# Kernel tuning notes

Hardware: AMD Instinct MI355X
Metric: run time of the kernel (lower is better)

Reference implementation:

```python
import jax, jax.numpy as jnp
import numpy as np

IN_FEATURES = 4096
OUT_FEATURES = 4096
NNZ = 1677722  # round(0.1 * 4096 * 4096)
N_TOKENS = 8192


def setup_inputs() -> dict:
    key = jax.random.key(0)
    k1, k2, k3, k4 = jax.random.split(key, 4)
    inputs = jax.random.normal(k1, (N_TOKENS, IN_FEATURES), dtype=jnp.float32)
    bound = 1.0 / IN_FEATURES ** 0.5
    weights = jax.random.uniform(k2, (NNZ,), minval=-bound, maxval=bound, dtype=jnp.float32)
    bias = jax.random.uniform(k3, (OUT_FEATURES,), minval=-bound, maxval=bound, dtype=jnp.float32)
    # COO indices: row (output) and col (input) indices, sampled like np.random.choice
    flat = jax.random.randint(k4, (NNZ,), 0, IN_FEATURES * OUT_FEATURES)
    row_ind = flat // IN_FEATURES
    col_ind = flat % IN_FEATURES
    indices = jnp.stack((row_ind, col_ind)).astype(jnp.int64)
    return {"inputs": inputs, "weights": weights, "bias": bias, "indices": indices}


def reference(inputs, weights, bias, indices):
    # Densify COO weight (duplicates are summed, matching torch coalesce/to_dense)
    dense_w = jnp.zeros((OUT_FEATURES, IN_FEATURES), dtype=weights.dtype)
    dense_w = dense_w.at[indices[0], indices[1]].add(weights)
    # output = (W @ x^T)^T + b  ==  x @ W^T + b
    out = jnp.einsum('ni,oi->no', inputs, dense_w) + bias
    return out
```

## Files before the change

### kernel.cpp

```cpp
#include <hip/hip_runtime.h>

#define M_TOK 8192
#define NF    4096
#define KF    4096
#define BK    64

typedef __attribute__((ext_vector_type(8))) short bf16x8;
typedef __attribute__((ext_vector_type(4))) float f32x4;
typedef __attribute__((ext_vector_type(2))) short s16x2;

__device__ __forceinline__ unsigned short f2bf(float f) {
    unsigned u = __builtin_bit_cast(unsigned, f);
    u += 0x7FFFu + ((u >> 16) & 1u);
    return (unsigned short)(u >> 16);
}

__device__ __forceinline__ float bf2f(unsigned short b) {
    unsigned u = ((unsigned)b) << 16;
    return __builtin_bit_cast(float, u);
}

__device__ __forceinline__ void load_lds16(const unsigned short* g, unsigned short* l) {
    __builtin_amdgcn_global_load_lds(
        (const __attribute__((address_space(1))) unsigned int*)g,
        (__attribute__((address_space(3))) unsigned int*)l,
        16, 0, 0);
}

__global__ void prep_zero_convx(const float4* __restrict__ X, ushort4* __restrict__ Xb,
                                uint4* __restrict__ Wb, int nx4, int nwb) {
    int i = blockIdx.x * blockDim.x + threadIdx.x;
    if (i < nwb) Wb[i] = (uint4){0u, 0u, 0u, 0u};
    if (i < nx4) {
        float4 v = X[i];
        ushort4 o;
        o.x = f2bf(v.x); o.y = f2bf(v.y); o.z = f2bf(v.z); o.w = f2bf(v.w);
        Xb[i] = o;
    }
}

__global__ void scatter_bf16(const int* __restrict__ idx, const float* __restrict__ w,
                             unsigned short* __restrict__ Wb, int nnz) {
    int t = blockIdx.x * blockDim.x + threadIdx.x;
    if (t >= nnz) return;
    int r = idx[t];
    int c = idx[nnz + t];
    size_t elem = (size_t)r * KF + c;
#if __has_builtin(__builtin_amdgcn_global_atomic_fadd_v2bf16)
    unsigned short wb = f2bf(w[t]);
    s16x2 val;
    if (elem & 1) { val[0] = 0; val[1] = (short)wb; }
    else          { val[0] = (short)wb; val[1] = 0; }
    __builtin_amdgcn_global_atomic_fadd_v2bf16(
        (__attribute__((address_space(1))) s16x2*)(Wb + (elem & ~(size_t)1)), val);
#else
    unsigned* addr = (unsigned*)(Wb + (elem & ~(size_t)1));
    float wf = w[t];
    unsigned old = __hip_atomic_load(addr, __ATOMIC_RELAXED, __HIP_MEMORY_SCOPE_AGENT), assumed;
    do {
        assumed = old;
        unsigned short cur = (elem & 1) ? (unsigned short)(assumed >> 16)
                                        : (unsigned short)(assumed & 0xffffu);
        unsigned short nw = f2bf(bf2f(cur) + wf);
        unsigned newv = (elem & 1) ? ((assumed & 0x0000ffffu) | ((unsigned)nw << 16))
                                   : ((assumed & 0xffff0000u) | (unsigned)nw);
        old = atomicCAS(addr, assumed, newv);
    } while (old != assumed);
#endif
}

__global__ __launch_bounds__(256) void gemm_bt_bias(
    const unsigned short* __restrict__ A,
    const unsigned short* __restrict__ B,
    const float* __restrict__ bias,
    float* __restrict__ C)
{
    __shared__ unsigned short As[128 * BK];
    __shared__ unsigned short Bs[128 * BK];

    const int tid  = threadIdx.x;
    const int lane = tid & 63;
    const int wave = tid >> 6;
    const int wm   = wave >> 1;
    const int wn   = wave & 1;
    const int bm   = blockIdx.x;
    const int bn   = blockIdx.y;

    f32x4 acc[4][4] = {};

    const int lr8 = lane >> 3;
    const int lp  = lane & 7;
    const int gc  = lp ^ lr8;

    const unsigned short* gA[4];
    const unsigned short* gB[4];
#pragma unroll
    for (int t = 0; t < 4; ++t) {
        int r = wave * 32 + t * 8 + lr8;
        gA[t] = A + (size_t)(bm * 128 + r) * KF + gc * 8;
        gB[t] = B + (size_t)(bn * 128 + r) * KF + gc * 8;
    }
    unsigned short* lA[4];
    unsigned short* lB[4];
#pragma unroll
    for (int t = 0; t < 4; ++t) {
        lA[t] = &As[(wave * 32 + t * 8) * BK];
        lB[t] = &Bs[(wave * 32 + t * 8) * BK];
    }

    const int fr   = lane & 15;
    const int quad = lane >> 4;
    int offA[4][2], offB[4][2];
#pragma unroll
    for (int i = 0; i < 4; ++i) {
        int rA = wm * 64 + i * 16 + fr;
        int rB = wn * 64 + i * 16 + fr;
#pragma unroll
        for (int s = 0; s < 2; ++s) {
            int c = s * 4 + quad;
            offA[i][s] = rA * BK + ((c ^ (rA & 7)) * 8);
            offB[i][s] = rB * BK + ((c ^ (rB & 7)) * 8);
        }
    }

    for (int k0 = 0; k0 < KF; k0 += BK) {
        __syncthreads();
#pragma unroll
        for (int t = 0; t < 4; ++t) load_lds16(gA[t], lA[t]);
#pragma unroll
        for (int t = 0; t < 4; ++t) load_lds16(gB[t], lB[t]);
#pragma unroll
        for (int t = 0; t < 4; ++t) { gA[t] += BK; gB[t] += BK; }
        __syncthreads();

#pragma unroll
        for (int s = 0; s < 2; ++s) {
            bf16x8 af[4], bfr[4];
#pragma unroll
            for (int i = 0; i < 4; ++i) af[i]  = *(const bf16x8*)&As[offA[i][s]];
#pragma unroll
            for (int j = 0; j < 4; ++j) bfr[j] = *(const bf16x8*)&Bs[offB[j][s]];
#pragma unroll
            for (int i = 0; i < 4; ++i)
#pragma unroll
                for (int j = 0; j < 4; ++j)
                    acc[i][j] = __builtin_amdgcn_mfma_f32_16x16x32_bf16(af[i], bfr[j], acc[i][j], 0, 0, 0);
        }
    }

    const int crow = bm * 128 + wm * 64;
    const int ccol = bn * 128 + wn * 64;
    const int c_l  = lane & 15;
    const int r_l  = (lane >> 4) * 4;
#pragma unroll
    for (int j = 0; j < 4; ++j) {
        int col = ccol + j * 16 + c_l;
        float bv = bias[col];
#pragma unroll
        for (int i = 0; i < 4; ++i) {
#pragma unroll
            for (int r = 0; r < 4; ++r)
                C[(size_t)(crow + i * 16 + r_l + r) * NF + col] = acc[i][j][r] + bv;
        }
    }
}

extern "C" void kernel_launch(void* const* d_in, const int* in_sizes, int n_in,
                              void* d_out, int out_size, void* d_ws, size_t ws_size,
                              hipStream_t stream) {
    const float* x    = (const float*)d_in[0];
    const float* w    = (const float*)d_in[1];
    const float* bias = (const float*)d_in[2];
    const int*   idx  = (const int*)d_in[3];
    float* out = (float*)d_out;
    const int nnz = in_sizes[1];

    unsigned short* Wb = (unsigned short*)d_ws;
    unsigned short* Xb = (unsigned short*)((char*)d_ws + (size_t)NF * KF * sizeof(unsigned short));

    const int nx4 = M_TOK * KF / 4;
    const int nwb = NF * KF * 2 / 16;

    prep_zero_convx<<<(nx4 + 255) / 256, 256, 0, stream>>>(
        (const float4*)x, (ushort4*)Xb, (uint4*)Wb, nx4, nwb);
    scatter_bf16<<<(nnz + 255) / 256, 256, 0, stream>>>(idx, w, Wb, nnz);
    gemm_bt_bias<<<dim3(M_TOK / 128, NF / 128), 256, 0, stream>>>(Xb, Wb, bias, out);
}
```

Baseline: 594.3 us.

## Rewrite GEMM as 256x256 tile, 8-wave, double-buffered LDS pipeline with block swizzle

Replaces the 128x128, 4-wave, single-buffered GEMM with a 256x256 tile computed by 8 waves, each holding 8x4 MFMA accumulators. Global-to-LDS loads for the next K tile are interleaved with MFMA work on the current buffer using explicit vmcnt waits, raw barriers and s_setprio. A grid swizzle is added for L2 locality. The aim is to hide load latency and raise arithmetic intensity, at the cost of 128KB LDS per block, heavy register pressure and fragile hand-written synchronization.

```diff
diff --git a/kernel.cpp b/kernel.cpp
--- a/kernel.cpp
+++ b/kernel.cpp
@@ -4,6 +4,7 @@
 #define NF    4096
 #define KF    4096
 #define BK    64
+#define NT    (KF / BK)
 
 typedef __attribute__((ext_vector_type(8))) short bf16x8;
 typedef __attribute__((ext_vector_type(4))) float f32x4;
@@ -26,6 +27,14 @@
         (__attribute__((address_space(3))) unsigned int*)l,
         16, 0, 0);
 }
+
+__device__ __forceinline__ void block_bar() {
+    asm volatile("" ::: "memory");
+    __builtin_amdgcn_s_barrier();
+    asm volatile("" ::: "memory");
+}
+
+#define VMCNT(n) asm volatile("s_waitcnt vmcnt(" #n ")" ::: "memory")
 
 __global__ void prep_zero_convx(const float4* __restrict__ X, ushort4* __restrict__ Xb,
                                 uint4* __restrict__ Wb, int nx4, int nwb) {
@@ -69,95 +78,147 @@
 #endif
 }
 
-__global__ __launch_bounds__(256) void gemm_bt_bias(
+__global__ __launch_bounds__(512, 2) void gemm_bt_bias(
     const unsigned short* __restrict__ A,
     const unsigned short* __restrict__ B,
     const float* __restrict__ bias,
     float* __restrict__ C)
 {
-    __shared__ unsigned short As[128 * BK];
-    __shared__ unsigned short Bs[128 * BK];
+    __shared__ unsigned short lds_u[65536];
+    char* const ldsb = (char*)lds_u;
 
     const int tid  = threadIdx.x;
     const int lane = tid & 63;
     const int wave = tid >> 6;
-    const int wm   = wave >> 1;
-    const int wn   = wave & 1;
-    const int bm   = blockIdx.x;
-    const int bn   = blockIdx.y;
-
-    f32x4 acc[4][4] = {};
-
-    const int lr8 = lane >> 3;
-    const int lp  = lane & 7;
-    const int gc  = lp ^ lr8;
-
-    const unsigned short* gA[4];
-    const unsigned short* gB[4];
-#pragma unroll
-    for (int t = 0; t < 4; ++t) {
-        int r = wave * 32 + t * 8 + lr8;
-        gA[t] = A + (size_t)(bm * 128 + r) * KF + gc * 8;
-        gB[t] = B + (size_t)(bn * 128 + r) * KF + gc * 8;
-    }
-    unsigned short* lA[4];
-    unsigned short* lB[4];
-#pragma unroll
-    for (int t = 0; t < 4; ++t) {
-        lA[t] = &As[(wave * 32 + t * 8) * BK];
-        lB[t] = &Bs[(wave * 32 + t * 8) * BK];
-    }
-
-    const int fr   = lane & 15;
-    const int quad = lane >> 4;
-    int offA[4][2], offB[4][2];
-#pragma unroll
-    for (int i = 0; i < 4; ++i) {
-        int rA = wm * 64 + i * 16 + fr;
-        int rB = wn * 64 + i * 16 + fr;
-#pragma unroll
-        for (int s = 0; s < 2; ++s) {
-            int c = s * 4 + quad;
-            offA[i][s] = rA * BK + ((c ^ (rA & 7)) * 8);
-            offB[i][s] = rB * BK + ((c ^ (rB & 7)) * 8);
-        }
-    }
-
-    for (int k0 = 0; k0 < KF; k0 += BK) {
-        __syncthreads();
-#pragma unroll
-        for (int t = 0; t < 4; ++t) load_lds16(gA[t], lA[t]);
-#pragma unroll
-        for (int t = 0; t < 4; ++t) load_lds16(gB[t], lB[t]);
-#pragma unroll
-        for (int t = 0; t < 4; ++t) { gA[t] += BK; gB[t] += BK; }
-        __syncthreads();
-
-#pragma unroll
-        for (int s = 0; s < 2; ++s) {
-            bf16x8 af[4], bfr[4];
-#pragma unroll
-            for (int i = 0; i < 4; ++i) af[i]  = *(const bf16x8*)&As[offA[i][s]];
-#pragma unroll
-            for (int j = 0; j < 4; ++j) bfr[j] = *(const bf16x8*)&Bs[offB[j][s]];
-#pragma unroll
-            for (int i = 0; i < 4; ++i)
-#pragma unroll
-                for (int j = 0; j < 4; ++j)
-                    acc[i][j] = __builtin_amdgcn_mfma_f32_16x16x32_bf16(af[i], bfr[j], acc[i][j], 0, 0, 0);
-        }
-    }
-
-    const int crow = bm * 128 + wm * 64;
-    const int ccol = bn * 128 + wn * 64;
-    const int c_l  = lane & 15;
-    const int r_l  = (lane >> 4) * 4;
+    const int wm   = wave >> 2;
+    const int wn   = wave & 3;
+
+    const int flat = blockIdx.y * 32 + blockIdx.x;
+    const int swz  = (flat & 7) * 64 + (flat >> 3);
+    const int bm   = swz & 31;
+    const int bn   = swz >> 5;
+
+    f32x4 acc[8][4] = {};
+
+    const int gc   = (lane & 3) ^ ((lane >> 3) & 3);
+    const int srow = wave * 16 + (lane >> 2);
+    const unsigned short* gA   = A + (size_t)(bm * 256 + srow) * KF + gc * 8;
+    const unsigned short* gB   = B + (size_t)(bn * 256 + srow) * KF + gc * 8;
+    const unsigned short* gAHi = gA + (size_t)128 * KF;
+    const unsigned short* gBHi = gB + (size_t)128 * KF;
+
+    unsigned short* const sdus = lds_u + wave * 512;
+
+    const int fr    = lane & 15;
+    const int quad  = lane >> 4;
+    const int pos16 = (quad ^ ((fr >> 1) & 3)) << 4;
+    const int rdA   = (wm * 128 + fr) * 64 + pos16;
+    const int rdB   = 32768 + (wn * 64 + fr) * 64 + pos16;
+
+#define STAGE(gp, gpHi, region, pbuf, h) do { \
+    load_lds16((gp)   + (h) * 32, sdus + (((pbuf) * 65536 + (region) + (h) * 16384       ) >> 1)); \
+    load_lds16((gpHi) + (h) * 32, sdus + (((pbuf) * 65536 + (region) + (h) * 16384 + 8192) >> 1)); \
+} while (0)
+
+#define RD_A4(dst, pbuf, h, i0) do { \
+    _Pragma("unroll") \
+    for (int _i = 0; _i < 4; ++_i) \
+        dst[_i] = *(const bf16x8*)(ldsb + (pbuf) * 65536 + (h) * 16384 + rdA + ((i0) + _i) * 1024); \
+} while (0)
+
+#define RD_B4(dst, pbuf, h) do { \
+    _Pragma("unroll") \
+    for (int _j = 0; _j < 4; ++_j) \
+        dst[_j] = *(const bf16x8*)(ldsb + (pbuf) * 65536 + (h) * 16384 + rdB + _j * 1024); \
+} while (0)
+
+#define MFMA16(i0, af, bfv) do { \
+    _Pragma("unroll") \
+    for (int _i = 0; _i < 4; ++_i) \
+        _Pragma("unroll") \
+        for (int _j = 0; _j < 4; ++_j) \
+            acc[(i0) + _i][_j] = __builtin_amdgcn_mfma_f32_16x16x32_bf16(af[_i], bfv[_j], acc[(i0) + _i][_j], 0, 0, 0); \
+} while (0)
+
+    STAGE(gA, gAHi, 0,     0, 0);
+    STAGE(gB, gBHi, 32768, 0, 0);
+    STAGE(gA, gAHi, 0,     0, 1);
+    STAGE(gB, gBHi, 32768, 0, 1);
+    gA += BK; gB += BK; gAHi += BK; gBHi += BK;
+    VMCNT(4);
+    block_bar();
+
+    int pb = 0;
+#pragma unroll 1
+    for (int t = 0; t < NT - 1; ++t) {
+        const int nb = pb ^ 1;
+        bf16x8 a[4], b[4];
+        RD_A4(a, pb, 0, 0);
+        RD_B4(b, pb, 0);
+        STAGE(gA, gAHi, 0, nb, 0);
+        block_bar();
+        __builtin_amdgcn_s_setprio(1);
+        MFMA16(0, a, b);
+        __builtin_amdgcn_s_setprio(0);
+        block_bar();
+        RD_A4(a, pb, 0, 4);
+        STAGE(gB, gBHi, 32768, nb, 0);
+        block_bar();
+        __builtin_amdgcn_s_setprio(1);
+        MFMA16(4, a, b);
+        __builtin_amdgcn_s_setprio(0);
+        VMCNT(4);
+        block_bar();
+        RD_A4(a, pb, 1, 0);
+        RD_B4(b, pb, 1);
+        STAGE(gA, gAHi, 0, nb, 1);
+        block_bar();
+        __builtin_amdgcn_s_setprio(1);
+        MFMA16(0, a, b);
+        __builtin_amdgcn_s_setprio(0);
+        block_bar();
+        RD_A4(a, pb, 1, 4);
+        STAGE(gB, gBHi, 32768, nb, 1);
+        block_bar();
+        __builtin_amdgcn_s_setprio(1);
+        MFMA16(4, a, b);
+        __builtin_amdgcn_s_setprio(0);
+        VMCNT(4);
+        block_bar();
+        gA += BK; gB += BK; gAHi += BK; gBHi += BK;
+        pb = nb;
+    }
+
+    {
+        bf16x8 a[4], b[4];
+        RD_A4(a, pb, 0, 0);
+        RD_B4(b, pb, 0);
+        MFMA16(0, a, b);
+        RD_A4(a, pb, 0, 4);
+        MFMA16(4, a, b);
+        VMCNT(0);
+        block_bar();
+        RD_A4(a, pb, 1, 0);
+        RD_B4(b, pb, 1);
+        MFMA16(0, a, b);
+        RD_A4(a, pb, 1, 4);
+        MFMA16(4, a, b);
+    }
+
+#undef STAGE
+#undef RD_A4
+#undef RD_B4
+#undef MFMA16
+
+    const int crow = bm * 256 + wm * 128;
+    const int ccol = bn * 256 + wn * 64;
+    const int r_l  = quad * 4;
 #pragma unroll
     for (int j = 0; j < 4; ++j) {
-        int col = ccol + j * 16 + c_l;
+        int col = ccol + j * 16 + fr;
         float bv = bias[col];
 #pragma unroll
-        for (int i = 0; i < 4; ++i) {
+        for (int i = 0; i < 8; ++i) {
 #pragma unroll
             for (int r = 0; r < 4; ++r)
                 C[(size_t)(crow + i * 16 + r_l + r) * NF + col] = acc[i][j][r] + bv;
@@ -184,5 +245,5 @@
     prep_zero_convx<<<(nx4 + 255) / 256, 256, 0, stream>>>(
         (const float4*)x, (ushort4*)Xb, (uint4*)Wb, nx4, nwb);
     scatter_bf16<<<(nnz + 255) / 256, 256, 0, stream>>>(idx, w, Wb, nnz);
-    gemm_bt_bias<<<dim3(M_TOK / 128, NF / 128), 256, 0, stream>>>(Xb, Wb, bias, out);
-}
+    gemm_bt_bias<<<dim3(32, 16), 512, 0, stream>>>(Xb, Wb, bias, out);
+}
```

Result: faster. 554.0 us (-6.8%).
